# Performance work log

Measured on AMD Instinct MI355X. Metric: run time of the kernel, lower is better.

## Reference

```python
import jax, jax.numpy as jnp
import numpy as np

D_MODEL = 1024
NUM_HEADS = 16
D_K = D_MODEL // NUM_HEADS


def setup_inputs() -> dict:
    key = jax.random.key(0)
    ks = jax.random.split(key, 11)
    B, S, D = 2, 2048, D_MODEL
    s = 1.0 / np.sqrt(D)
    return {
        "Q": jax.random.normal(ks[0], (B, S, D), jnp.float32),
        "K": jax.random.normal(ks[1], (B, S, D), jnp.float32),
        "V": jax.random.normal(ks[2], (B, S, D), jnp.float32),
        "Wq": jax.random.normal(ks[3], (D, D), jnp.float32) * s,
        "bq": jax.random.normal(ks[4], (D,), jnp.float32) * s,
        "Wk": jax.random.normal(ks[5], (D, D), jnp.float32) * s,
        "bk": jax.random.normal(ks[6], (D,), jnp.float32) * s,
        "Wv": jax.random.normal(ks[7], (D, D), jnp.float32) * s,
        "bv": jax.random.normal(ks[8], (D,), jnp.float32) * s,
        "Wo": jax.random.normal(ks[9], (D, D), jnp.float32) * s,
        "bo": jax.random.normal(ks[10], (D,), jnp.float32) * s,
    }


def _split_heads(x):
    B, S, D = x.shape
    return x.reshape(B, S, NUM_HEADS, D_K).transpose(0, 2, 1, 3)  # [B,H,S,d_k]


def reference(Q, K, V, Wq, bq, Wk, bk, Wv, bv, Wo, bo):
    q = _split_heads(Q @ Wq + bq)
    k = _split_heads(K @ Wk + bk)
    v = _split_heads(V @ Wv + bv)
    scale = 1.0 / np.sqrt(D_K)
    scores = jnp.einsum('bhqd,bhkd->bhqk', q, k) * scale
    P = jax.nn.softmax(scores, axis=-1)  # max-subtract + exp + normalize
    O = jnp.einsum('bhqk,bhkd->bhqd', P, v)
    B, H, S, dk = O.shape
    O = O.transpose(0, 2, 1, 3).reshape(B, S, H * dk)
    return O @ Wo + bo
```

## Files before the change

### kernel.cpp

```cpp
#include <hip/hip_runtime.h>
#include <math.h>

#define S_LEN 2048
#define DMODEL 1024
#define NHEADS 16
#define DK 64

#define QSCALE 0.1803368801111244f

typedef __attribute__((ext_vector_type(8))) _Float16 f16x8;
typedef __attribute__((ext_vector_type(2))) __fp16 hf16x2;
typedef __attribute__((ext_vector_type(4))) float f32x4;

static __device__ __forceinline__ unsigned short f2h(float f) {
    _Float16 h = (_Float16)f;
    return __builtin_bit_cast(unsigned short, h);
}

static __device__ __forceinline__ unsigned pack2(float a, float b) {
    hf16x2 h = __builtin_amdgcn_cvt_pkrtz(a, b);
    return __builtin_bit_cast(unsigned, h);
}

static __device__ __forceinline__ void gload16(const void* g, void* l) {
    __builtin_amdgcn_global_load_lds(
        (const __attribute__((address_space(1))) void*)g,
        (__attribute__((address_space(3))) void*)l, 16, 0, 0);
}

__global__ __launch_bounds__(256)
void wprep_kernel(const float* __restrict__ w0, const float* __restrict__ w1,
                  const float* __restrict__ w2, const float* __restrict__ w3,
                  unsigned short* __restrict__ wt)
{
    __shared__ float tile[64][65];
    const int z = blockIdx.z;
    const float* W = z == 0 ? w0 : (z == 1 ? w1 : (z == 2 ? w2 : w3));
    unsigned short* Wt = wt + (size_t)z * 1048576;
    const int k0 = blockIdx.x * 64, n0 = blockIdx.y * 64;
    const int t = threadIdx.x;
    #pragma unroll
    for (int i = 0; i < 4; ++i) {
        int idx = i * 256 + t;
        int r = idx >> 4, c4 = (idx & 15) * 4;
        float4 v = *reinterpret_cast<const float4*>(W + (size_t)(k0 + r) * 1024 + n0 + c4);
        tile[r][c4 + 0] = v.x; tile[r][c4 + 1] = v.y;
        tile[r][c4 + 2] = v.z; tile[r][c4 + 3] = v.w;
    }
    __syncthreads();
    #pragma unroll
    for (int i = 0; i < 4; ++i) {
        int idx = i * 256 + t;
        int nr = idx >> 4, kc4 = (idx & 15) * 4;
        ushort4 h;
        h.x = f2h(tile[kc4 + 0][nr]); h.y = f2h(tile[kc4 + 1][nr]);
        h.z = f2h(tile[kc4 + 2][nr]); h.w = f2h(tile[kc4 + 3][nr]);
        *reinterpret_cast<ushort4*>(Wt + (size_t)(n0 + nr) * 1024 + k0 + kc4) = h;
    }
}

__global__ __launch_bounds__(512)
void proj_gemm_kernel(const float* __restrict__ x0, const float* __restrict__ x1,
                      const float* __restrict__ x2,
                      const unsigned short* __restrict__ wt_base,
                      const float* __restrict__ b0, const float* __restrict__ b1,
                      const float* __restrict__ b2,
                      unsigned short* __restrict__ dst_base)
{
    __shared__ char Als[16384];
    __shared__ char Bls[16384];

    const int z = blockIdx.z;
    const float* Ag = z == 0 ? x0 : (z == 1 ? x1 : x2);
    const char* Bg = (const char*)(wt_base + (size_t)z * 1048576);
    const float* bias = z == 0 ? b0 : (z == 1 ? b1 : b2);
    const int mode = z;

    const int tid = threadIdx.x;
    const int w = tid >> 6, l = tid & 63, a = l & 15, g = l >> 4;
    const int wm = w >> 2, wn = w & 3;
    const int ntile = blockIdx.y & 7;
    const int mtile = blockIdx.x + ((blockIdx.y >> 3) << 3);
    const int bm = mtile * 128, bn = ntile * 128;

    const int arow = tid >> 2;
    const int ac16 = tid & 3;
    const int aswz = (arow & 7) << 4;
    const int srow = tid >> 3;
    const int sc8 = tid & 7;

    f32x4 acc[4][2] = {};

    for (int ks = 0; ks < 16; ++ks) {
        const float* ap = Ag + (size_t)(bm + arow) * 1024 + ks * 64 + 16 * ac16;
        float4 a0 = reinterpret_cast<const float4*>(ap)[0];
        float4 a1 = reinterpret_cast<const float4*>(ap)[1];
        float4 a2 = reinterpret_cast<const float4*>(ap)[2];
        float4 a3 = reinterpret_cast<const float4*>(ap)[3];

        #pragma unroll
        for (int it = 0; it < 2; ++it) {
            const int row = it * 64 + srow;
            const int gc = (sc8 << 4) ^ ((row & 7) << 4);
            gload16(Bg + (size_t)(bn + row) * 2048 + ks * 128 + gc,
                    &Bls[(size_t)(it * 512 + tid) * 16]);
        }

        uint4 w0, w1;
        w0.x = pack2(a0.x, a0.y); w0.y = pack2(a0.z, a0.w);
        w0.z = pack2(a1.x, a1.y); w0.w = pack2(a1.z, a1.w);
        w1.x = pack2(a2.x, a2.y); w1.y = pack2(a2.z, a2.w);
        w1.z = pack2(a3.x, a3.y); w1.w = pack2(a3.z, a3.w);
        const int abase = arow * 128;
        const int aoff = 32 * ac16;
        *reinterpret_cast<uint4*>(&Als[abase + (aoff ^ aswz)]) = w0;
        *reinterpret_cast<uint4*>(&Als[abase + ((aoff + 16) ^ aswz)]) = w1;

        __syncthreads();
        #pragma unroll
        for (int kc = 0; kc < 2; ++kc) {
            f16x8 af[4], bf[2];
            #pragma unroll
            for (int mi = 0; mi < 4; ++mi) {
                const int row = wm * 64 + 16 * mi + a;
                af[mi] = *reinterpret_cast<const f16x8*>(
                    &Als[row * 128 + ((kc * 64 + g * 16) ^ ((row & 7) << 4))]);
            }
            #pragma unroll
            for (int ni = 0; ni < 2; ++ni) {
                const int row = wn * 32 + 16 * ni + a;
                bf[ni] = *reinterpret_cast<const f16x8*>(
                    &Bls[row * 128 + ((kc * 64 + g * 16) ^ ((row & 7) << 4))]);
            }
            __builtin_amdgcn_s_setprio(1);
            #pragma unroll
            for (int mi = 0; mi < 4; ++mi)
                #pragma unroll
                for (int ni = 0; ni < 2; ++ni)
                    acc[mi][ni] = __builtin_amdgcn_mfma_f32_16x16x32_f16(
                        af[mi], bf[ni], acc[mi][ni], 0, 0, 0);
            __builtin_amdgcn_s_setprio(0);
        }
        __syncthreads();
    }

    unsigned short* mydst = dst_base + (size_t)z * 4194304;

    #pragma unroll
    for (int ni = 0; ni < 2; ++ni) {
        const int n = bn + wn * 32 + 16 * ni + a;
        const float bv = bias[n];
        #pragma unroll
        for (int mi = 0; mi < 4; ++mi) {
            const int mbase = bm + wm * 64 + 16 * mi + g * 4;
            if (mode == 2) {
                const int b = mbase >> 11, s = mbase & (S_LEN - 1);
                const int h = n >> 6, d = n & (DK - 1);
                ushort4 st;
                st.x = f2h(acc[mi][ni][0] + bv);
                st.y = f2h(acc[mi][ni][1] + bv);
                st.z = f2h(acc[mi][ni][2] + bv);
                st.w = f2h(acc[mi][ni][3] + bv);
                *reinterpret_cast<ushort4*>(
                    mydst + ((size_t)((b * NHEADS + h) * DK + d)) * S_LEN + s) = st;
            } else {
                const float sc = (mode == 0) ? QSCALE : 1.0f;
                #pragma unroll
                for (int r = 0; r < 4; ++r) {
                    const int m = mbase + r;
                    const int b = m >> 11, s = m & (S_LEN - 1);
                    const int h = n >> 6, d = n & (DK - 1);
                    mydst[((size_t)((b * NHEADS + h) * S_LEN + s)) * DK + d] =
                        f2h((acc[mi][ni][r] + bv) * sc);
                }
            }
        }
    }
}

__global__ __launch_bounds__(512)
void out_gemm_kernel(const unsigned short* __restrict__ Agh,
                     const unsigned short* __restrict__ Bgh,
                     const float* __restrict__ bias, float* __restrict__ out)
{
    __shared__ char Als[16384];
    __shared__ char Bls[16384];

    const char* Ag = (const char*)Agh;
    const char* Bg = (const char*)Bgh;

    const int tid = threadIdx.x;
    const int w = tid >> 6, l = tid & 63, a = l & 15, g = l >> 4;
    const int wm = w >> 2, wn = w & 3;
    const int ntile = blockIdx.y & 7;
    const int mtile = blockIdx.x + ((blockIdx.y >> 3) << 3);
    const int bm = mtile * 128, bn = ntile * 128;

    const int srow = tid >> 3;
    const int sc8 = tid & 7;

    f32x4 acc[4][2] = {};

    for (int k0b = 0; k0b < 2048; k0b += 128) {
        #pragma unroll
        for (int it = 0; it < 2; ++it) {
            const int row = it * 64 + srow;
            const int gc = (sc8 << 4) ^ ((row & 7) << 4);
            gload16(Ag + (size_t)(bm + row) * 2048 + k0b + gc,
                    &Als[(size_t)(it * 512 + tid) * 16]);
            gload16(Bg + (size_t)(bn + row) * 2048 + k0b + gc,
                    &Bls[(size_t)(it * 512 + tid) * 16]);
        }
        __syncthreads();
        #pragma unroll
        for (int kc = 0; kc < 2; ++kc) {
            f16x8 af[4], bf[2];
            #pragma unroll
            for (int mi = 0; mi < 4; ++mi) {
                const int row = wm * 64 + 16 * mi + a;
                af[mi] = *reinterpret_cast<const f16x8*>(
                    &Als[row * 128 + ((kc * 64 + g * 16) ^ ((row & 7) << 4))]);
            }
            #pragma unroll
            for (int ni = 0; ni < 2; ++ni) {
                const int row = wn * 32 + 16 * ni + a;
                bf[ni] = *reinterpret_cast<const f16x8*>(
                    &Bls[row * 128 + ((kc * 64 + g * 16) ^ ((row & 7) << 4))]);
            }
            __builtin_amdgcn_s_setprio(1);
            #pragma unroll
            for (int mi = 0; mi < 4; ++mi)
                #pragma unroll
                for (int ni = 0; ni < 2; ++ni)
                    acc[mi][ni] = __builtin_amdgcn_mfma_f32_16x16x32_f16(
                        af[mi], bf[ni], acc[mi][ni], 0, 0, 0);
            __builtin_amdgcn_s_setprio(0);
        }
        __syncthreads();
    }

    #pragma unroll
    for (int ni = 0; ni < 2; ++ni) {
        const int n = bn + wn * 32 + 16 * ni + a;
        const float bv = bias[n];
        #pragma unroll
        for (int mi = 0; mi < 4; ++mi) {
            const int mbase = bm + wm * 64 + 16 * mi + g * 4;
            #pragma unroll
            for (int r = 0; r < 4; ++r)
                out[(size_t)(mbase + r) * 1024 + n] = acc[mi][ni][r] + bv;
        }
    }
}

__global__ __launch_bounds__(512, 4)
void attn_mfma_kernel(const unsigned short* __restrict__ qb,
                      const unsigned short* __restrict__ kb,
                      const unsigned short* __restrict__ vt,
                      unsigned short* __restrict__ ob)
{
    __shared__ char Kls[2][2][8192];
    __shared__ char Vls[2][8192];
    __shared__ unsigned short Pl[8][16][72];

    const int tid = threadIdx.x;
    const int w = tid >> 6;
    const int p = w >> 2;
    const int wsub = w & 3;
    const int l = tid & 63;
    const int a = l & 15;
    const int g = l >> 4;
    const int bh = blockIdx.y;
    const int q0 = blockIdx.x * 128 + wsub * 32;

    const unsigned short* qhead = qb + (size_t)bh * S_LEN * DK;
    const char* khead = (const char*)(kb + (size_t)bh * S_LEN * DK);
    const char* vhead = (const char*)(vt + (size_t)bh * DK * S_LEN);

    f16x8 qf[2][2];
    #pragma unroll
    for (int j = 0; j < 2; ++j)
        #pragma unroll
        for (int c = 0; c < 2; ++c)
            qf[j][c] = *reinterpret_cast<const f16x8*>(
                qhead + (size_t)(q0 + 16 * j + a) * DK + 32 * c + 8 * g);

    f16x8 onesf;
    #pragma unroll
    for (int i = 0; i < 8; ++i) onesf[i] = (_Float16)1.f;

    f32x4 oacc[4][2] = {};
    f32x4 lacc[2] = {};
    float mrun[2] = {-INFINITY, -INFINITY};

    const int sgrow = w * 8 + (l >> 3);
    const int sgc = ((l & 7) << 4) ^ ((sgrow & 7) << 4);

    #define STAGE_K(gg)                                                        \
        do {                                                                   \
            _Pragma("unroll")                                                  \
            for (int t = 0; t < 2; ++t)                                        \
                gload16(khead + (size_t)((2 * (gg) + t) * 64 + sgrow) * 128 + sgc, \
                        &Kls[(gg) & 1][t][(size_t)w * 1024]);                  \
        } while (0)
    #define STAGE_V(gg)                                                        \
        do {                                                                   \
            _Pragma("unroll")                                                  \
            for (int t = 0; t < 2; ++t)                                        \
                gload16(vhead + (size_t)sgrow * 4096 + (size_t)(2 * (gg) + t) * 128 + sgc, \
                        &Vls[t][(size_t)w * 1024]);                            \
        } while (0)

    STAGE_K(0);

    for (int i = 0; i < 16; ++i) {
        __syncthreads();

        STAGE_V(i);
        if (i < 15) STAGE_K(i + 1);

        const char* Kbuf = Kls[i & 1][p];
        f16x8 kf[2][4];
        #pragma unroll
        for (int c = 0; c < 2; ++c)
            #pragma unroll
            for (int T = 0; T < 4; ++T) {
                const int row = 16 * T + a;
                kf[c][T] = *reinterpret_cast<const f16x8*>(
                    &Kbuf[row * 128 + ((64 * c + 16 * g) ^ ((row & 7) << 4))]);
            }

        f32x4 sacc[4][2] = {};
        __builtin_amdgcn_s_setprio(1);
        #pragma unroll
        for (int c = 0; c < 2; ++c)
            #pragma unroll
            for (int T = 0; T < 4; ++T)
                #pragma unroll
                for (int j = 0; j < 2; ++j)
                    sacc[T][j] = __builtin_amdgcn_mfma_f32_16x16x32_f16(
                        kf[c][T], qf[j][c], sacc[T][j], 0, 0, 0);
        __builtin_amdgcn_s_setprio(0);

        float pr1[4][4];
        #pragma unroll
        for (int j = 0; j < 2; ++j) {
            float lm = -INFINITY;
            #pragma unroll
            for (int T = 0; T < 4; ++T)
                #pragma unroll
                for (int r = 0; r < 4; ++r) lm = fmaxf(lm, sacc[T][j][r]);

            if (!__all(lm <= mrun[j] + 8.f)) {
                float vmax = fmaxf(lm, __shfl_xor(lm, 16));
                vmax = fmaxf(vmax, __shfl_xor(vmax, 32));
                const float mnew = fmaxf(mrun[j], vmax);
                const float corr = __builtin_amdgcn_exp2f(mrun[j] - mnew);
                #pragma unroll
                for (int t = 0; t < 4; ++t) {
                    oacc[t][j][0] *= corr; oacc[t][j][1] *= corr;
                    oacc[t][j][2] *= corr; oacc[t][j][3] *= corr;
                }
                lacc[j][0] *= corr; lacc[j][1] *= corr;
                lacc[j][2] *= corr; lacc[j][3] *= corr;
                mrun[j] = mnew;
            }

            const float mj = mrun[j];
            if (j == 0) {
                #pragma unroll
                for (int T = 0; T < 4; ++T) {
                    float e0 = __builtin_amdgcn_exp2f(sacc[T][0][0] - mj);
                    float e1 = __builtin_amdgcn_exp2f(sacc[T][0][1] - mj);
                    float e2 = __builtin_amdgcn_exp2f(sacc[T][0][2] - mj);
                    float e3 = __builtin_amdgcn_exp2f(sacc[T][0][3] - mj);
                    unsigned* dst = reinterpret_cast<unsigned*>(&Pl[w][a][16 * T + 4 * g]);
                    dst[0] = pack2(e0, e1);
                    dst[1] = pack2(e2, e3);
                }
            } else {
                #pragma unroll
                for (int T = 0; T < 4; ++T)
                    #pragma unroll
                    for (int r = 0; r < 4; ++r)
                        pr1[T][r] = __builtin_amdgcn_exp2f(sacc[T][1][r] - mj);
            }
        }

        if (i < 15) {
            asm volatile("s_waitcnt vmcnt(2)" ::: "memory");
        } else {
            asm volatile("s_waitcnt vmcnt(0)" ::: "memory");
        }

        const char* Vbuf = Vls[p];
        f16x8 vf[2][4];
        #pragma unroll
        for (int c = 0; c < 2; ++c)
            #pragma unroll
            for (int t = 0; t < 4; ++t) {
                const int row = 16 * t + a;
                vf[c][t] = *reinterpret_cast<const f16x8*>(
                    &Vbuf[row * 128 + ((64 * c + 16 * g) ^ ((row & 7) << 4))]);
            }

        #pragma unroll
        for (int c = 0; c < 2; ++c) {
            f16x8 pf = *reinterpret_cast<const f16x8*>(&Pl[w][a][32 * c + 8 * g]);
            __builtin_amdgcn_s_setprio(1);
            #pragma unroll
            for (int t = 0; t < 4; ++t)
                oacc[t][0] = __builtin_amdgcn_mfma_f32_16x16x32_f16(
                    vf[c][t], pf, oacc[t][0], 0, 0, 0);
            lacc[0] = __builtin_amdgcn_mfma_f32_16x16x32_f16(
                onesf, pf, lacc[0], 0, 0, 0);
            __builtin_amdgcn_s_setprio(0);
        }

        #pragma unroll
        for (int T = 0; T < 4; ++T) {
            unsigned* dst = reinterpret_cast<unsigned*>(&Pl[w][a][16 * T + 4 * g]);
            dst[0] = pack2(pr1[T][0], pr1[T][1]);
            dst[1] = pack2(pr1[T][2], pr1[T][3]);
        }
        #pragma unroll
        for (int c = 0; c < 2; ++c) {
            f16x8 pf = *reinterpret_cast<const f16x8*>(&Pl[w][a][32 * c + 8 * g]);
            __builtin_amdgcn_s_setprio(1);
            #pragma unroll
            for (int t = 0; t < 4; ++t)
                oacc[t][1] = __builtin_amdgcn_mfma_f32_16x16x32_f16(
                    vf[c][t], pf, oacc[t][1], 0, 0, 0);
            lacc[1] = __builtin_amdgcn_mfma_f32_16x16x32_f16(
                onesf, pf, lacc[1], 0, 0, 0);
            __builtin_amdgcn_s_setprio(0);
        }
    }
    #undef STAGE_K
    #undef STAGE_V

    __syncthreads();
    float* Ob = (float*)Kls;
    float* Ml = (float*)Vls;
    if (p == 1) {
        #pragma unroll
        for (int j = 0; j < 2; ++j) {
            if (g == 0) {
                Ml[((wsub * 2 + j) * 2 + 0) * 16 + a] = mrun[j];
                Ml[((wsub * 2 + j) * 2 + 1) * 16 + a] = lacc[j][0];
            }
            #pragma unroll
            for (int t = 0; t < 4; ++t)
                #pragma unroll
                for (int r = 0; r < 4; ++r)
                    Ob[((wsub * 2 + j) * 64 + 16 * t + 4 * g + r) * 16 + a] =
                        oacc[t][j][r];
        }
    }
    __syncthreads();
    if (p == 0) {
        const int b = bh >> 4;
        const int h = bh & (NHEADS - 1);
        #pragma unroll
        for (int j = 0; j < 2; ++j) {
            const float m1 = Ml[((wsub * 2 + j) * 2 + 0) * 16 + a];
            const float l1 = Ml[((wsub * 2 + j) * 2 + 1) * 16 + a];
            const float m0 = mrun[j];
            const float ms = fmaxf(m0, m1);
            const float c0 = __builtin_amdgcn_exp2f(m0 - ms);
            const float c1 = __builtin_amdgcn_exp2f(m1 - ms);
            const float inv = 1.f / (lacc[j][0] * c0 + l1 * c1);
            unsigned short* dst0 =
                ob + (size_t)(b * S_LEN + q0 + 16 * j + a) * DMODEL + h * DK;
            #pragma unroll
            for (int t = 0; t < 4; ++t) {
                ushort4 st;
                #pragma unroll
                for (int r = 0; r < 4; ++r) {
                    const float o1 =
                        Ob[((wsub * 2 + j) * 64 + 16 * t + 4 * g + r) * 16 + a];
                    const float val = (oacc[t][j][r] * c0 + o1 * c1) * inv;
                    ((unsigned short*)&st)[r] = f2h(val);
                }
                *reinterpret_cast<ushort4*>(dst0 + 16 * t + 4 * g) = st;
            }
        }
    }
}

extern "C" void kernel_launch(void* const* d_in, const int* in_sizes, int n_in,
                              void* d_out, int out_size, void* d_ws, size_t ws_size,
                              hipStream_t stream)
{
    const float* Q  = (const float*)d_in[0];
    const float* K  = (const float*)d_in[1];
    const float* V  = (const float*)d_in[2];
    const float* Wq = (const float*)d_in[3];
    const float* bq = (const float*)d_in[4];
    const float* Wk = (const float*)d_in[5];
    const float* bk = (const float*)d_in[6];
    const float* Wv = (const float*)d_in[7];
    const float* bv = (const float*)d_in[8];
    const float* Wo = (const float*)d_in[9];
    const float* bo = (const float*)d_in[10];
    float* out = (float*)d_out;

    unsigned short* xh  = (unsigned short*)d_ws;
    unsigned short* wt  = xh + (size_t)3 * 4194304;
    unsigned short* qb  = wt + (size_t)4 * 1048576;
    unsigned short* kb  = qb + 4194304;
    unsigned short* vtb = kb + 4194304;
    unsigned short* obh = vtb + 4194304;

    wprep_kernel<<<dim3(16, 16, 4), 256, 0, stream>>>(Wq, Wk, Wv, Wo, wt);

    proj_gemm_kernel<<<dim3(8, 32, 3), 512, 0, stream>>>(
        Q, K, V, wt, bq, bk, bv, qb);

    attn_mfma_kernel<<<dim3(S_LEN / 128, 2 * NHEADS), 512, 0, stream>>>(qb, kb, vtb, obh);

    out_gemm_kernel<<<dim3(8, 32, 1), 512, 0, stream>>>(
        obh, wt + (size_t)3 * 1048576, bo, out);
}
```

Baseline: 130.8 us.

## Single-buffer K/V tiles and prefetch both during the PV phase

Replaces the double-buffered K staging and separate V staging with one combined stage that loads the K and V tiles for both key halves into single buffers. The next iteration's loads are issued after the current V fragments are in registers, so they overlap only the PV MFMAs, with barriers around them. This cuts shared-memory use per block, which may allow more resident blocks per CU. The trade-off is an extra barrier per iteration and less prefetch distance, so the QK step may stall on loads. The epilogue is rearranged to reuse the smaller K, V and P buffers for the cross-half reduction.

```diff
diff --git a/kernel.cpp b/kernel.cpp
--- a/kernel.cpp
+++ b/kernel.cpp
@@ -259,7 +259,7 @@
                       const unsigned short* __restrict__ vt,
                       unsigned short* __restrict__ ob)
 {
-    __shared__ char Kls[2][2][8192];
+    __shared__ char Kls[2][8192];
     __shared__ char Vls[2][8192];
     __shared__ unsigned short Pl[8][16][72];
 
@@ -293,33 +293,22 @@
     f32x4 lacc[2] = {};
     float mrun[2] = {-INFINITY, -INFINITY};
 
-    const int sgrow = w * 8 + (l >> 3);
-    const int sgc = ((l & 7) << 4) ^ ((sgrow & 7) << 4);
-
-    #define STAGE_K(gg)                                                        \
-        do {                                                                   \
-            _Pragma("unroll")                                                  \
-            for (int t = 0; t < 2; ++t)                                        \
-                gload16(khead + (size_t)((2 * (gg) + t) * 64 + sgrow) * 128 + sgc, \
-                        &Kls[(gg) & 1][t][(size_t)w * 1024]);                  \
+    const int srow = tid >> 3;
+    const int sgc = ((tid & 7) << 4) ^ ((srow & 7) << 4);
+
+    #define STAGE1(t2)                                                          \
+        do {                                                                    \
+            gload16(khead + (size_t)((t2) * 64 + srow) * 128 + sgc,             \
+                    &Kls[(t2) & 1][(size_t)w * 1024]);                          \
+            gload16(vhead + (size_t)srow * 4096 + (size_t)(t2) * 128 + sgc,     \
+                    &Vls[(t2) & 1][(size_t)w * 1024]);                          \
         } while (0)
-    #define STAGE_V(gg)                                                        \
-        do {                                                                   \
-            _Pragma("unroll")                                                  \
-            for (int t = 0; t < 2; ++t)                                        \
-                gload16(vhead + (size_t)sgrow * 4096 + (size_t)(2 * (gg) + t) * 128 + sgc, \
-                        &Vls[t][(size_t)w * 1024]);                            \
-        } while (0)
-
-    STAGE_K(0);
+
+    STAGE1(0);
+    STAGE1(1);
+    __syncthreads();
 
     for (int i = 0; i < 16; ++i) {
-        __syncthreads();
-
-        STAGE_V(i);
-        if (i < 15) STAGE_K(i + 1);
-
-        const char* Kbuf = Kls[i & 1][p];
         f16x8 kf[2][4];
         #pragma unroll
         for (int c = 0; c < 2; ++c)
@@ -327,7 +316,7 @@
             for (int T = 0; T < 4; ++T) {
                 const int row = 16 * T + a;
                 kf[c][T] = *reinterpret_cast<const f16x8*>(
-                    &Kbuf[row * 128 + ((64 * c + 16 * g) ^ ((row & 7) << 4))]);
+                    &Kls[p][row * 128 + ((64 * c + 16 * g) ^ ((row & 7) << 4))]);
             }
 
         f32x4 sacc[4][2] = {};
@@ -387,13 +376,6 @@
             }
         }
 
-        if (i < 15) {
-            asm volatile("s_waitcnt vmcnt(2)" ::: "memory");
-        } else {
-            asm volatile("s_waitcnt vmcnt(0)" ::: "memory");
-        }
-
-        const char* Vbuf = Vls[p];
         f16x8 vf[2][4];
         #pragma unroll
         for (int c = 0; c < 2; ++c)
@@ -401,8 +383,14 @@
             for (int t = 0; t < 4; ++t) {
                 const int row = 16 * t + a;
                 vf[c][t] = *reinterpret_cast<const f16x8*>(
-                    &Vbuf[row * 128 + ((64 * c + 16 * g) ^ ((row & 7) << 4))]);
-            }
+                    &Vls[p][row * 128 + ((64 * c + 16 * g) ^ ((row & 7) << 4))]);
+            }
+
+        __syncthreads();
+        if (i < 15) {
+            STAGE1(2 * i + 2);
+            STAGE1(2 * i + 3);
+        }
 
         #pragma unroll
         for (int c = 0; c < 2; ++c) {
@@ -435,16 +423,17 @@
                 onesf, pf, lacc[1], 0, 0, 0);
             __builtin_amdgcn_s_setprio(0);
         }
-    }
-    #undef STAGE_K
-    #undef STAGE_V
-
-    __syncthreads();
-    float* Ob = (float*)Kls;
-    float* Ml = (float*)Vls;
+        __syncthreads();
+    }
+    #undef STAGE1
+
+    float* Ob0 = (float*)Kls;
+    float* Ob1 = (float*)Vls;
+    float* Ml  = (float*)Pl;
     if (p == 1) {
         #pragma unroll
         for (int j = 0; j < 2; ++j) {
+            float* Ob = j ? Ob1 : Ob0;
             if (g == 0) {
                 Ml[((wsub * 2 + j) * 2 + 0) * 16 + a] = mrun[j];
                 Ml[((wsub * 2 + j) * 2 + 1) * 16 + a] = lacc[j][0];
@@ -453,8 +442,7 @@
             for (int t = 0; t < 4; ++t)
                 #pragma unroll
                 for (int r = 0; r < 4; ++r)
-                    Ob[((wsub * 2 + j) * 64 + 16 * t + 4 * g + r) * 16 + a] =
-                        oacc[t][j][r];
+                    Ob[(wsub * 64 + 16 * t + 4 * g + r) * 16 + a] = oacc[t][j][r];
         }
     }
     __syncthreads();
@@ -463,6 +451,7 @@
         const int h = bh & (NHEADS - 1);
         #pragma unroll
         for (int j = 0; j < 2; ++j) {
+            const float* Ob = j ? Ob1 : Ob0;
             const float m1 = Ml[((wsub * 2 + j) * 2 + 0) * 16 + a];
             const float l1 = Ml[((wsub * 2 + j) * 2 + 1) * 16 + a];
             const float m0 = mrun[j];
@@ -477,8 +466,7 @@
                 ushort4 st;
                 #pragma unroll
                 for (int r = 0; r < 4; ++r) {
-                    const float o1 =
-                        Ob[((wsub * 2 + j) * 64 + 16 * t + 4 * g + r) * 16 + a];
+                    const float o1 = Ob[(wsub * 64 + 16 * t + 4 * g + r) * 16 + a];
                     const float val = (oacc[t][j][r] * c0 + o1 * c1) * inv;
                     ((unsigned short*)&st)[r] = f2h(val);
                 }
```

After: 145.0 us. 1.11x slower.
